# Kernel tuning notes

Measured on AMD Instinct MI355X. Metric: run time of the kernel, lower is better.

Reference implementation:

```python
import jax, jax.numpy as jnp
from jax import lax
import numpy as np

B, C_IN, C_OUT, H, W = 16, 64, 64, 160, 160
K, STRIDE, PAD, DIL, SHIFT = 3, 1, 1, 1, 1


def setup_inputs() -> dict:
    key = jax.random.key(0)
    kx, kw = jax.random.split(key)
    x = jax.random.normal(kx, (B, C_IN, H, W), dtype=jnp.float32)
    weight = jax.random.normal(kw, (C_OUT, C_IN, K, K), dtype=jnp.float32)
    return {"x": x, "weight": weight}


def reference(x, weight):
    Bn, C, Hh, Ww = x.shape
    # zero-pad spatially by shift_distance on all sides (matches F.pad)
    xp = jnp.pad(x, ((0, 0), (0, 0), (SHIFT, SHIFT), (SHIFT, SHIFT)))
    Hp, Wp = Hh + 2 * SHIFT, Ww + 2 * SHIFT
    # shifts list: (dx, dy) for channel groups c % 5
    dxs = jnp.array([0, SHIFT, 0, -SHIFT, 0])
    dys = jnp.array([0, 0, SHIFT, 0, -SHIFT])
    cmod = jnp.arange(C) % 5
    dy = dys[cmod]  # [C] roll along H (dim 2)
    dx = dxs[cmod]  # [C] roll along W (dim 3)
    # torch.roll semantics: out[h, w] = in[(h - dy) % Hp, (w - dx) % Wp]
    row = (jnp.arange(Hp)[None, :] - dy[:, None]) % Hp  # [C, Hp]
    col = (jnp.arange(Wp)[None, :] - dx[:, None]) % Wp  # [C, Wp]
    # single fused gather over channel-dependent row/col indices
    x_shifted = xp[:, jnp.arange(C)[:, None, None], row[:, :, None], col[:, None, :]]
    out = lax.conv_general_dilated(
        x_shifted, weight,
        window_strides=(STRIDE, STRIDE),
        padding=((PAD, PAD), (PAD, PAD)),
        rhs_dilation=(DIL, DIL),
        dimension_numbers=("NCHW", "OIHW", "NCHW"),
    )
    # crop the extra border introduced by the pre-pad
    return out[:, :, 1:-1, 1:-1]
```

## Files before the change

### kernel.cpp

```cpp
#include <hip/hip_runtime.h>
#include <hip/hip_bf16.h>

#define BATCH 16
#define CIN 64
#define COUT 64
#define HH 160
#define WW 160
#define HP 162
#define WP 162

#define ABUF 21760
#define PSTR 161

typedef __attribute__((ext_vector_type(8))) __bf16 bf16x8;
typedef __attribute__((ext_vector_type(4))) float f32x4;
typedef __attribute__((ext_vector_type(8))) unsigned short ushort8;

typedef __attribute__((address_space(1))) const unsigned int gu32;
typedef __attribute__((address_space(3))) unsigned int lu32;

__global__ __launch_bounds__(256) void prep(const float* __restrict__ x,
                                            const float* __restrict__ w,
                                            unsigned short* __restrict__ xs,
                                            unsigned short* __restrict__ wb) {
  __shared__ float lds[64 * PSTR];

  if (blockIdx.x >= BATCH * HP) {
    int e = (blockIdx.x - BATCH * HP) * 256 + threadIdx.x;
    if (e < 9 * 64 * 64) {
      int tap = e >> 12;
      int o = (e >> 6) & 63;
      int c = e & 63;
      float v = w[((size_t)(o * 64 + c)) * 9 + tap];
      __hip_bfloat16 h = __float2bfloat16(v);
      wb[e] = *reinterpret_cast<unsigned short*>(&h);
    }
    return;
  }

  int y = blockIdx.x % HP;
  int b = blockIdx.x / HP;
  int tid = threadIdx.x;

#pragma unroll
  for (int it = 0; it < 10; ++it) {
    int idx = it * 256 + tid;
    int c = idx / 40;
    int j = idx - c * 40;
    int cm = c % 5;
    int dy = (cm == 2) ? 1 : ((cm == 4) ? -1 : 0);
    int yy = y - dy;
    f32x4 v = {0.f, 0.f, 0.f, 0.f};
    if (yy >= 1 && yy <= HH)
      v = *reinterpret_cast<const f32x4*>(
          x + (((size_t)(b * CIN + c)) * HH + (size_t)(yy - 1)) * WW + j * 4);
    int p0 = c * PSTR + 4 * j;
#pragma unroll
    for (int e = 0; e < 4; ++e) lds[p0 + e] = v[e];
  }
  __syncthreads();

  int cg = tid & 7;
  int xr = tid >> 3;
  int dxe[8], rowb[8];
#pragma unroll
  for (int e = 0; e < 8; ++e) {
    int c = cg * 8 + e;
    int cm = c % 5;
    dxe[e] = (cm == 1) ? 1 : ((cm == 3) ? -1 : 0);
    rowb[e] = c * PSTR;
  }
  size_t obase = ((size_t)(b * HP + y) * WP) * CIN + cg * 8;
#pragma unroll
  for (int it = 0; it < 6; ++it) {
    int xi = it * 32 + xr;
    if (xi < WP) {
      ushort8 val;
#pragma unroll
      for (int e = 0; e < 8; ++e) {
        int xx = xi - dxe[e] - 1;
        float v = 0.f;
        if (xx >= 0 && xx < WW) v = lds[rowb[e] + xx];
        __hip_bfloat16 h = __float2bfloat16(v);
        val[e] = *reinterpret_cast<unsigned short*>(&h);
      }
      *reinterpret_cast<ushort8*>(xs + obase + (size_t)xi * CIN) = val;
    }
  }
}

__global__ __launch_bounds__(512, 1) void conv_mfma(const unsigned short* __restrict__ xs,
                                                    const unsigned short* __restrict__ wb,
                                                    float* __restrict__ out) {
  __shared__ __align__(16) unsigned short lds_a[ABUF];
  __shared__ __align__(16) unsigned short lds_b[ABUF];
  __shared__ __align__(16) unsigned short lds_w[9 * 64 * 64];

  int tid = threadIdx.x;
  int blk = blockIdx.x;
  int tile0 = (blk & 7) * 32 + (blk >> 3);
  int ntiles = (tile0 < 64) ? 7 : 6;

  int wv = tid >> 6;
  int lane = tid & 63;
  int l15 = lane & 15;
  int q = lane >> 4;

  int goff[6];
#pragma unroll
  for (int r = 0; r < 6; ++r) {
    int u = r * 512 + tid;
    int p = u >> 3;
    int j = (u & 7) ^ (p & 7);
    int pr = p / 34, pc = p - pr * 34;
    goff[r] = (pr * WP + pc) * CIN + j * 8;
  }

  int bw0 = l15 * 64 + ((q ^ (l15 & 7)) * 8);
  int bw1 = l15 * 64 + (((4 + q) ^ (l15 & 7)) * 8);

#define STAGE_TO(BUFARR, T_)                                                   \
  {                                                                            \
    int sb_ = (T_) / 100;                                                      \
    int srr_ = (T_) - sb_ * 100;                                               \
    int sti_ = srr_ / 5, stj_ = srr_ - sti_ * 5;                               \
    const unsigned short* srcb_ = xs +                                         \
        ((size_t)sb_ * HP + (size_t)(sti_ * 8)) * WP * CIN +                   \
        (size_t)(stj_ * 32) * CIN;                                             \
    unsigned short* dst0_ = (BUFARR) + wv * 512;                               \
    _Pragma("unroll") for (int r = 0; r < 5; ++r)                              \
        __builtin_amdgcn_global_load_lds((gu32*)(srcb_ + goff[r]),             \
                                         (lu32*)(dst0_ + r * 4096), 16, 0, 0); \
    if (tid < 160)                                                             \
      __builtin_amdgcn_global_load_lds((gu32*)(srcb_ + goff[5]),               \
                                       (lu32*)(dst0_ + 5 * 4096), 16, 0, 0);   \
  }

#define LOAD_A(RBUF, bufp, tt)                                                 \
  {                                                                            \
    const int ch_ = (tt) / 9, ky_ = ((tt) % 9) / 3, kx_ = (tt) % 3;            \
    _Pragma("unroll") for (int mt = 0; mt < 2; ++mt) {                         \
      int pix = (wv + ky_) * 34 + kx_ + l15 + mt * 16;                         \
      int chunk = (ch_ * 4 + q) ^ (pix & 7);                                   \
      Ab[bufp][mt] =                                                           \
          *reinterpret_cast<const bf16x8*>(&(RBUF)[pix * 64 + chunk * 8]);     \
    }                                                                          \
  }

#define LOAD_BW(bufp, tt)                                                      \
  {                                                                            \
    const int ch_ = (tt) / 9, tap_ = (tt) % 9;                                 \
    _Pragma("unroll") for (int nt = 0; nt < 4; ++nt)                           \
        Bb[bufp][nt] = *reinterpret_cast<const bf16x8*>(                       \
            &lds_w[tap_ * 4096 + nt * 1024 + (ch_ ? bw1 : bw0)]);              \
  }

#define TILE_BODY(I_, RBUF, WBUF)                                              \
  {                                                                            \
    int t_ = tile0 + 256 * (I_);                                               \
    int b_ = t_ / 100;                                                         \
    int rr_ = t_ - b_ * 100;                                                   \
    int ti_ = rr_ / 5, tj_ = rr_ - ti_ * 5;                                    \
    int y0_ = ti_ * 8, x0_ = tj_ * 32;                                         \
    if ((I_) + 1 < ntiles) STAGE_TO(WBUF, tile0 + 256 * ((I_) + 1));           \
    _Pragma("unroll") for (int a_ = 0; a_ < 2; ++a_)                           \
      _Pragma("unroll") for (int c2_ = 0; c2_ < 4; ++c2_)                      \
        acc[a_][c2_] = (f32x4){0.f, 0.f, 0.f, 0.f};                            \
    LOAD_A(RBUF, 0, 0);                                                        \
    LOAD_BW(0, 0);                                                             \
    _Pragma("unroll") for (int tt = 0; tt < 18; ++tt) {                        \
      if (tt + 1 < 18) {                                                       \
        LOAD_A(RBUF, (tt + 1) & 1, tt + 1);                                    \
        LOAD_BW((tt + 1) & 1, tt + 1);                                         \
      }                                                                        \
      __builtin_amdgcn_s_setprio(1);                                           \
      _Pragma("unroll") for (int mt = 0; mt < 2; ++mt)                         \
        _Pragma("unroll") for (int nt = 0; nt < 4; ++nt)                       \
          acc[mt][nt] = __builtin_amdgcn_mfma_f32_16x16x32_bf16(               \
              Ab[tt & 1][mt], Bb[tt & 1][nt], acc[mt][nt], 0, 0, 0);           \
      __builtin_amdgcn_s_setprio(0);                                           \
    }                                                                          \
    __syncthreads();                                                           \
    _Pragma("unroll") for (int mt = 0; mt < 2; ++mt) {                         \
      int orow_ = y0_ + wv;                                                    \
      int xo_ = x0_ + mt * 16 + q * 4;                                         \
      _Pragma("unroll") for (int nt = 0; nt < 4; ++nt) {                       \
        int o_ = nt * 16 + l15;                                                \
        *reinterpret_cast<f32x4*>(                                             \
            out + ((size_t)(b_ * COUT + o_) * HH + (size_t)orow_) * WW + xo_) = \
            acc[mt][nt];                                                       \
      }                                                                        \
    }                                                                          \
  }

  f32x4 acc[2][4];
  bf16x8 Ab[2][2];
  bf16x8 Bb[2][4];

#pragma unroll
  for (int r = 0; r < 9; ++r) {
    int u = r * 512 + tid;
    int orow = u >> 3;
    int jj = (u & 7) ^ (orow & 7);
    __builtin_amdgcn_global_load_lds((gu32*)(wb + orow * 64 + jj * 8),
                                     (lu32*)(lds_w + (u & ~63) * 8), 16, 0, 0);
  }
  STAGE_TO(lds_a, tile0);
  __syncthreads();

  for (int i = 0; i < ntiles; i += 2) {
    TILE_BODY(i, lds_a, lds_b);
    if (i + 1 < ntiles) TILE_BODY(i + 1, lds_b, lds_a);
  }

#undef TILE_BODY
#undef LOAD_BW
#undef LOAD_A
#undef STAGE_TO
}

extern "C" void kernel_launch(void* const* d_in, const int* in_sizes, int n_in,
                              void* d_out, int out_size, void* d_ws, size_t ws_size,
                              hipStream_t stream) {
  const float* x = (const float*)d_in[0];
  const float* w = (const float*)d_in[1];
  float* out = (float*)d_out;

  unsigned short* xs = (unsigned short*)d_ws;
  unsigned short* wb = (unsigned short*)((char*)d_ws + (size_t)BATCH * HP * WP * CIN * 2);

  hipLaunchKernelGGL(prep, dim3(BATCH * HP + 144), dim3(256), 0, stream, x, w, xs, wb);
  hipLaunchKernelGGL(conv_mfma, dim3(256), dim3(512), 0, stream, xs, wb, out);
}
```

Measured before the change: 232.0 us.

## Keep weights register-resident and remap waves to 2 rows x 32 output channels

Drops the LDS copy of the weights. Each wave now holds its half of the output channels (18 taps x 2 bf16x8 fragments) in registers, loaded once from global memory. The wave-to-output mapping changes from 1 row x 64 channels to 2 rows x 32 channels, so per-step LDS traffic is only the activation fragments. LDS use shrinks and launch_bounds asks for 2 blocks per CU. The trade-off is much higher register pressure from 36 persistent B vectors plus accumulators, which may cause spills or defeat the occupancy goal.

```diff
diff --git a/kernel.cpp b/kernel.cpp
--- a/kernel.cpp
+++ b/kernel.cpp
@@ -89,12 +89,11 @@
   }
 }
 
-__global__ __launch_bounds__(512, 1) void conv_mfma(const unsigned short* __restrict__ xs,
+__global__ __launch_bounds__(512, 2) void conv_mfma(const unsigned short* __restrict__ xs,
                                                     const unsigned short* __restrict__ wb,
                                                     float* __restrict__ out) {
   __shared__ __align__(16) unsigned short lds_a[ABUF];
   __shared__ __align__(16) unsigned short lds_b[ABUF];
-  __shared__ __align__(16) unsigned short lds_w[9 * 64 * 64];
 
   int tid = threadIdx.x;
   int blk = blockIdx.x;
@@ -102,6 +101,8 @@
   int ntiles = (tile0 < 64) ? 7 : 6;
 
   int wv = tid >> 6;
+  int rp = wv >> 1;
+  int nh = wv & 1;
   int lane = tid & 63;
   int l15 = lane & 15;
   int q = lane >> 4;
@@ -115,9 +116,6 @@
     int pr = p / 34, pc = p - pr * 34;
     goff[r] = (pr * WP + pc) * CIN + j * 8;
   }
-
-  int bw0 = l15 * 64 + ((q ^ (l15 & 7)) * 8);
-  int bw1 = l15 * 64 + (((4 + q) ^ (l15 & 7)) * 8);
 
 #define STAGE_TO(BUFARR, T_)                                                   \
   {                                                                            \
@@ -139,20 +137,13 @@
 #define LOAD_A(RBUF, bufp, tt)                                                 \
   {                                                                            \
     const int ch_ = (tt) / 9, ky_ = ((tt) % 9) / 3, kx_ = (tt) % 3;            \
-    _Pragma("unroll") for (int mt = 0; mt < 2; ++mt) {                         \
-      int pix = (wv + ky_) * 34 + kx_ + l15 + mt * 16;                         \
-      int chunk = (ch_ * 4 + q) ^ (pix & 7);                                   \
-      Ab[bufp][mt] =                                                           \
-          *reinterpret_cast<const bf16x8*>(&(RBUF)[pix * 64 + chunk * 8]);     \
-    }                                                                          \
-  }
-
-#define LOAD_BW(bufp, tt)                                                      \
-  {                                                                            \
-    const int ch_ = (tt) / 9, tap_ = (tt) % 9;                                 \
-    _Pragma("unroll") for (int nt = 0; nt < 4; ++nt)                           \
-        Bb[bufp][nt] = *reinterpret_cast<const bf16x8*>(                       \
-            &lds_w[tap_ * 4096 + nt * 1024 + (ch_ ? bw1 : bw0)]);              \
+    _Pragma("unroll") for (int rr = 0; rr < 2; ++rr)                           \
+      _Pragma("unroll") for (int mt = 0; mt < 2; ++mt) {                       \
+        int pix = (2 * rp + rr + ky_) * 34 + kx_ + l15 + mt * 16;              \
+        int chunk = (ch_ * 4 + q) ^ (pix & 7);                                 \
+        Ab[bufp][rr * 2 + mt] =                                                \
+            *reinterpret_cast<const bf16x8*>(&(RBUF)[pix * 64 + chunk * 8]);   \
+      }                                                                        \
   }
 
 #define TILE_BODY(I_, RBUF, WBUF)                                              \
@@ -163,49 +154,46 @@
     int ti_ = rr_ / 5, tj_ = rr_ - ti_ * 5;                                    \
     int y0_ = ti_ * 8, x0_ = tj_ * 32;                                         \
     if ((I_) + 1 < ntiles) STAGE_TO(WBUF, tile0 + 256 * ((I_) + 1));           \
-    _Pragma("unroll") for (int a_ = 0; a_ < 2; ++a_)                           \
-      _Pragma("unroll") for (int c2_ = 0; c2_ < 4; ++c2_)                      \
+    _Pragma("unroll") for (int a_ = 0; a_ < 4; ++a_)                           \
+      _Pragma("unroll") for (int c2_ = 0; c2_ < 2; ++c2_)                      \
         acc[a_][c2_] = (f32x4){0.f, 0.f, 0.f, 0.f};                            \
     LOAD_A(RBUF, 0, 0);                                                        \
-    LOAD_BW(0, 0);                                                             \
     _Pragma("unroll") for (int tt = 0; tt < 18; ++tt) {                        \
-      if (tt + 1 < 18) {                                                       \
-        LOAD_A(RBUF, (tt + 1) & 1, tt + 1);                                    \
-        LOAD_BW((tt + 1) & 1, tt + 1);                                         \
-      }                                                                        \
+      if (tt + 1 < 18) LOAD_A(RBUF, (tt + 1) & 1, tt + 1);                     \
       __builtin_amdgcn_s_setprio(1);                                           \
-      _Pragma("unroll") for (int mt = 0; mt < 2; ++mt)                         \
-        _Pragma("unroll") for (int nt = 0; nt < 4; ++nt)                       \
-          acc[mt][nt] = __builtin_amdgcn_mfma_f32_16x16x32_bf16(               \
-              Ab[tt & 1][mt], Bb[tt & 1][nt], acc[mt][nt], 0, 0, 0);           \
+      _Pragma("unroll") for (int am = 0; am < 4; ++am)                         \
+        _Pragma("unroll") for (int ns = 0; ns < 2; ++ns)                       \
+          acc[am][ns] = __builtin_amdgcn_mfma_f32_16x16x32_bf16(               \
+              Ab[tt & 1][am], Breg[tt][ns], acc[am][ns], 0, 0, 0);             \
       __builtin_amdgcn_s_setprio(0);                                           \
     }                                                                          \
     __syncthreads();                                                           \
-    _Pragma("unroll") for (int mt = 0; mt < 2; ++mt) {                         \
-      int orow_ = y0_ + wv;                                                    \
-      int xo_ = x0_ + mt * 16 + q * 4;                                         \
-      _Pragma("unroll") for (int nt = 0; nt < 4; ++nt) {                       \
-        int o_ = nt * 16 + l15;                                                \
-        *reinterpret_cast<f32x4*>(                                             \
-            out + ((size_t)(b_ * COUT + o_) * HH + (size_t)orow_) * WW + xo_) = \
-            acc[mt][nt];                                                       \
+    _Pragma("unroll") for (int rr2 = 0; rr2 < 2; ++rr2)                        \
+      _Pragma("unroll") for (int mt = 0; mt < 2; ++mt) {                       \
+        int orow_ = y0_ + 2 * rp + rr2;                                        \
+        int xo_ = x0_ + mt * 16 + q * 4;                                       \
+        _Pragma("unroll") for (int ns = 0; ns < 2; ++ns) {                     \
+          int o_ = nh * 32 + ns * 16 + l15;                                    \
+          *reinterpret_cast<f32x4*>(                                           \
+              out + ((size_t)(b_ * COUT + o_) * HH + (size_t)orow_) * WW +     \
+              xo_) = acc[rr2 * 2 + mt][ns];                                    \
+        }                                                                      \
       }                                                                        \
-    }                                                                          \
-  }
-
-  f32x4 acc[2][4];
-  bf16x8 Ab[2][2];
-  bf16x8 Bb[2][4];
-
-#pragma unroll
-  for (int r = 0; r < 9; ++r) {
-    int u = r * 512 + tid;
-    int orow = u >> 3;
-    int jj = (u & 7) ^ (orow & 7);
-    __builtin_amdgcn_global_load_lds((gu32*)(wb + orow * 64 + jj * 8),
-                                     (lu32*)(lds_w + (u & ~63) * 8), 16, 0, 0);
-  }
+  }
+
+  f32x4 acc[4][2];
+  bf16x8 Ab[2][4];
+  bf16x8 Breg[18][2];
+
   STAGE_TO(lds_a, tile0);
+#pragma unroll
+  for (int tt = 0; tt < 18; ++tt) {
+    const int ch_ = tt / 9, tap_ = tt % 9;
+#pragma unroll
+    for (int ns = 0; ns < 2; ++ns)
+      Breg[tt][ns] = *reinterpret_cast<const bf16x8*>(
+          wb + tap_ * 4096 + (nh * 2 + ns) * 1024 + l15 * 64 + ch_ * 32 + q * 8);
+  }
   __syncthreads();
 
   for (int i = 0; i < ntiles; i += 2) {
@@ -214,7 +202,6 @@
   }
 
 #undef TILE_BODY
-#undef LOAD_BW
 #undef LOAD_A
 #undef STAGE_TO
 }
```

Result: slower. 274.9 us (+18.5%).

## Split output channels across wave pairs using 1024-thread blocks

Applied to the files above, without the earlier changes.

Doubles the workgroup to 16 waves, with each pair of waves sharing an output row and each wave computing half of the 64 output channels. Per-wave accumulator and B-fragment registers are halved, and the staging and weight loads are redistributed over 1024 threads with bounds guards. The goal is more waves per CU to hide LDS and MFMA latency. In exchange, every A fragment is now read from LDS by two waves, and the per-tile __syncthreads spans twice as many waves.

```diff
diff --git a/kernel.cpp b/kernel.cpp
--- a/kernel.cpp
+++ b/kernel.cpp
@@ -89,9 +89,9 @@
   }
 }
 
-__global__ __launch_bounds__(512, 1) void conv_mfma(const unsigned short* __restrict__ xs,
-                                                    const unsigned short* __restrict__ wb,
-                                                    float* __restrict__ out) {
+__global__ __launch_bounds__(1024, 4) void conv_mfma(const unsigned short* __restrict__ xs,
+                                                     const unsigned short* __restrict__ wb,
+                                                     float* __restrict__ out) {
   __shared__ __align__(16) unsigned short lds_a[ABUF];
   __shared__ __align__(16) unsigned short lds_b[ABUF];
   __shared__ __align__(16) unsigned short lds_w[9 * 64 * 64];
@@ -102,14 +102,16 @@
   int ntiles = (tile0 < 64) ? 7 : 6;
 
   int wv = tid >> 6;
+  int rw = wv >> 1;
+  int nh = wv & 1;
   int lane = tid & 63;
   int l15 = lane & 15;
   int q = lane >> 4;
 
-  int goff[6];
-#pragma unroll
-  for (int r = 0; r < 6; ++r) {
-    int u = r * 512 + tid;
+  int goff[3];
+#pragma unroll
+  for (int r = 0; r < 3; ++r) {
+    int u = r * 1024 + tid;
     int p = u >> 3;
     int j = (u & 7) ^ (p & 7);
     int pr = p / 34, pc = p - pr * 34;
@@ -127,20 +129,20 @@
     const unsigned short* srcb_ = xs +                                         \
         ((size_t)sb_ * HP + (size_t)(sti_ * 8)) * WP * CIN +                   \
         (size_t)(stj_ * 32) * CIN;                                             \
-    unsigned short* dst0_ = (BUFARR) + wv * 512;                               \
-    _Pragma("unroll") for (int r = 0; r < 5; ++r)                              \
+    _Pragma("unroll") for (int r = 0; r < 3; ++r) {                            \
+      int u_ = r * 1024 + tid;                                                 \
+      if (u_ < 2720)                                                           \
         __builtin_amdgcn_global_load_lds((gu32*)(srcb_ + goff[r]),             \
-                                         (lu32*)(dst0_ + r * 4096), 16, 0, 0); \
-    if (tid < 160)                                                             \
-      __builtin_amdgcn_global_load_lds((gu32*)(srcb_ + goff[5]),               \
-                                       (lu32*)(dst0_ + 5 * 4096), 16, 0, 0);   \
+                                         (lu32*)((BUFARR) + (u_ & ~63) * 8),   \
+                                         16, 0, 0);                            \
+    }                                                                          \
   }
 
 #define LOAD_A(RBUF, bufp, tt)                                                 \
   {                                                                            \
     const int ch_ = (tt) / 9, ky_ = ((tt) % 9) / 3, kx_ = (tt) % 3;            \
     _Pragma("unroll") for (int mt = 0; mt < 2; ++mt) {                         \
-      int pix = (wv + ky_) * 34 + kx_ + l15 + mt * 16;                         \
+      int pix = (rw + ky_) * 34 + kx_ + l15 + mt * 16;                         \
       int chunk = (ch_ * 4 + q) ^ (pix & 7);                                   \
       Ab[bufp][mt] =                                                           \
           *reinterpret_cast<const bf16x8*>(&(RBUF)[pix * 64 + chunk * 8]);     \
@@ -150,9 +152,9 @@
 #define LOAD_BW(bufp, tt)                                                      \
   {                                                                            \
     const int ch_ = (tt) / 9, tap_ = (tt) % 9;                                 \
-    _Pragma("unroll") for (int nt = 0; nt < 4; ++nt)                           \
-        Bb[bufp][nt] = *reinterpret_cast<const bf16x8*>(                       \
-            &lds_w[tap_ * 4096 + nt * 1024 + (ch_ ? bw1 : bw0)]);              \
+    _Pragma("unroll") for (int ns = 0; ns < 2; ++ns)                           \
+        Bb[bufp][ns] = *reinterpret_cast<const bf16x8*>(                       \
+            &lds_w[tap_ * 4096 + (nh * 2 + ns) * 1024 + (ch_ ? bw1 : bw0)]);   \
   }
 
 #define TILE_BODY(I_, RBUF, WBUF)                                              \
@@ -164,7 +166,7 @@
     int y0_ = ti_ * 8, x0_ = tj_ * 32;                                         \
     if ((I_) + 1 < ntiles) STAGE_TO(WBUF, tile0 + 256 * ((I_) + 1));           \
     _Pragma("unroll") for (int a_ = 0; a_ < 2; ++a_)                           \
-      _Pragma("unroll") for (int c2_ = 0; c2_ < 4; ++c2_)                      \
+      _Pragma("unroll") for (int c2_ = 0; c2_ < 2; ++c2_)                      \
         acc[a_][c2_] = (f32x4){0.f, 0.f, 0.f, 0.f};                            \
     LOAD_A(RBUF, 0, 0);                                                        \
     LOAD_BW(0, 0);                                                             \
@@ -175,35 +177,37 @@
       }                                                                        \
       __builtin_amdgcn_s_setprio(1);                                           \
       _Pragma("unroll") for (int mt = 0; mt < 2; ++mt)                         \
-        _Pragma("unroll") for (int nt = 0; nt < 4; ++nt)                       \
-          acc[mt][nt] = __builtin_amdgcn_mfma_f32_16x16x32_bf16(               \
-              Ab[tt & 1][mt], Bb[tt & 1][nt], acc[mt][nt], 0, 0, 0);           \
+        _Pragma("unroll") for (int ns = 0; ns < 2; ++ns)                       \
+          acc[mt][ns] = __builtin_amdgcn_mfma_f32_16x16x32_bf16(               \
+              Ab[tt & 1][mt], Bb[tt & 1][ns], acc[mt][ns], 0, 0, 0);           \
       __builtin_amdgcn_s_setprio(0);                                           \
     }                                                                          \
     __syncthreads();                                                           \
     _Pragma("unroll") for (int mt = 0; mt < 2; ++mt) {                         \
-      int orow_ = y0_ + wv;                                                    \
+      int orow_ = y0_ + rw;                                                    \
       int xo_ = x0_ + mt * 16 + q * 4;                                         \
-      _Pragma("unroll") for (int nt = 0; nt < 4; ++nt) {                       \
-        int o_ = nt * 16 + l15;                                                \
+      _Pragma("unroll") for (int ns = 0; ns < 2; ++ns) {                       \
+        int o_ = nh * 32 + ns * 16 + l15;                                      \
         *reinterpret_cast<f32x4*>(                                             \
             out + ((size_t)(b_ * COUT + o_) * HH + (size_t)orow_) * WW + xo_) = \
-            acc[mt][nt];                                                       \
+            acc[mt][ns];                                                       \
       }                                                                        \
     }                                                                          \
   }
 
-  f32x4 acc[2][4];
+  f32x4 acc[2][2];
   bf16x8 Ab[2][2];
-  bf16x8 Bb[2][4];
-
-#pragma unroll
-  for (int r = 0; r < 9; ++r) {
-    int u = r * 512 + tid;
-    int orow = u >> 3;
-    int jj = (u & 7) ^ (orow & 7);
-    __builtin_amdgcn_global_load_lds((gu32*)(wb + orow * 64 + jj * 8),
-                                     (lu32*)(lds_w + (u & ~63) * 8), 16, 0, 0);
+  bf16x8 Bb[2][2];
+
+#pragma unroll
+  for (int r = 0; r < 5; ++r) {
+    int u = r * 1024 + tid;
+    if (u < 4608) {
+      int orow = u >> 3;
+      int jj = (u & 7) ^ (orow & 7);
+      __builtin_amdgcn_global_load_lds((gu32*)(wb + orow * 64 + jj * 8),
+                                       (lu32*)(lds_w + (u & ~63) * 8), 16, 0, 0);
+    }
   }
   STAGE_TO(lds_a, tile0);
   __syncthreads();
@@ -230,5 +234,5 @@
   unsigned short* wb = (unsigned short*)((char*)d_ws + (size_t)BATCH * HP * WP * CIN * 2);
 
   hipLaunchKernelGGL(prep, dim3(BATCH * HP + 144), dim3(256), 0, stream, x, w, xs, wb);
-  hipLaunchKernelGGL(conv_mfma, dim3(256), dim3(512), 0, stream, xs, wb, out);
+  hipLaunchKernelGGL(conv_mfma, dim3(256), dim3(1024), 0, stream, xs, wb, out);
 }
```

Result: faster. 226.2 us (-2.5%).
